# Optimization experiments

Measured on AMD Instinct MI355X. Metric: run time of the kernel, lower is better.

Reference implementation:

```python
import jax, jax.numpy as jnp
import numpy as np

B, N, C, E = 4, 20000, 64, 320000

def setup_inputs() -> dict:
    key = jax.random.key(0)
    ks = jax.random.split(key, 9)
    s = 0.1
    return {
        "x": jax.random.normal(ks[0], (B, N, C), jnp.float32),
        "edge_index": jax.random.randint(ks[1], (2, E), 0, N, jnp.int64),
        "lin_w": jax.random.normal(ks[2], (C, C), jnp.float32) * s,
        "bias": jnp.zeros((C,), jnp.float32),
        "up1_w": jax.random.normal(ks[3], (C, C), jnp.float32) * s,
        "up2_w": jax.random.normal(ks[4], (C, C), jnp.float32) * s,
        "lo1_w": jax.random.normal(ks[5], (C, C), jnp.float32) * s,
        "lo2_w": jax.random.normal(ks[6], (C, C), jnp.float32) * s,
        "last_w": jax.random.normal(ks[7], (2 * C, 2 * C), jnp.float32) * s,
    }

def reference(x, edge_index, lin_w, bias, up1_w, up2_w, lo1_w, lo2_w, last_w):
    n = x.shape[1]
    # add self loops (PyG add_self_loops)
    loops = jnp.arange(n, dtype=edge_index.dtype)
    row = jnp.concatenate([edge_index[0], loops])  # source
    col = jnp.concatenate([edge_index[1], loops])  # target
    # linear transform (Linear with no bias: x @ W^T)
    h = jnp.einsum("bnc,oc->bno", x, lin_w)
    # symmetric degree normalization; degree computed on col (targets)
    deg = jax.ops.segment_sum(jnp.ones_like(col, dtype=h.dtype), col, num_segments=n)
    dis = jnp.where(deg > 0, deg ** -0.5, 0.0)
    norm = dis[row] * dis[col]  # [E+N]
    # gather / scale / scatter-add (GCN propagate with aggr='add')
    msg = h[:, row, :] * norm[None, :, None]          # [B, E+N, C]
    agg = jax.ops.segment_sum(jnp.swapaxes(msg, 0, 1), col, num_segments=n)  # [N, B, C]
    out = jnp.swapaxes(agg, 0, 1) + bias              # [B, N, C]
    fst = jax.nn.sigmoid(out)
    upper = jnp.einsum("bnc,oc->bno", jnp.einsum("bnc,oc->bno", fst, up1_w), up2_w)
    lower = jnp.einsum("bnc,oc->bno", jnp.einsum("bnc,oc->bno", fst, lo1_w), lo2_w)
    combined = jnp.concatenate([upper, lower], axis=2)  # [B, N, 2C]
    last = jnp.einsum("bnc,oc->bno", combined, last_w)
    return jax.nn.relu(last)
```

## Files before the change

kernel.cpp:

```cpp
#include <hip/hip_runtime.h>
#include <cstdint>
#include <cstddef>

#define NODES 20000
#define NEDGE 320000
#define CAP 64
#define NEB 1250
#define LINB 16
#define BIGB 32

using bf16x8 = __attribute__((ext_vector_type(8))) __bf16;
using f32x4  = __attribute__((ext_vector_type(4))) float;
using f32x2  = __attribute__((ext_vector_type(2))) float;

__device__ __forceinline__ unsigned short f2bf(float f) {
  union { float f; unsigned int u; } v; v.f = f;
  unsigned int r = v.u + 0x7FFF + ((v.u >> 16) & 1);
  return (unsigned short)(r >> 16);
}

__global__ void k_build(const int* __restrict__ ei, int* __restrict__ cnt,
                        int* __restrict__ csr,
                        const float* __restrict__ lin, const float* __restrict__ u1,
                        const float* __restrict__ u2, const float* __restrict__ l1,
                        const float* __restrict__ l2, const float* __restrict__ lastw,
                        unsigned short* __restrict__ wb16) {
  __shared__ float tmp_u[4][64];
  __shared__ float tmp_l[4][64];
  int bid = blockIdx.x, t = threadIdx.x;
  if (bid < NEB) {
    int i = bid * 256 + t;
    if (i < NEDGE) {
      int row = ei[i];
      int col = ei[NEDGE + i];
      int pos = atomicAdd(&cnt[col], 1);
      if (pos < CAP) csr[col * CAP + pos] = row;
    }
  } else if (bid < NEB + LINB) {
    int g = (bid - NEB) * 256 + t;
    wb16[g] = f2bf(lin[g]);
  } else {
    int o0 = (bid - NEB - LINB) * 4;
    int ol = t >> 6, p = t & 63;
    float su = 0.f, sl = 0.f;
    for (int k = 0; k < 64; ++k) {
      float lu = lastw[(o0 + ol) * 128 + k];
      float ll = lastw[(o0 + ol) * 128 + 64 + k];
      su += lu * u2[k * 64 + p];
      sl += ll * l2[k * 64 + p];
    }
    tmp_u[ol][p] = su;
    tmp_l[ol][p] = sl;
    __syncthreads();
    int j = p;
    float acc = 0.f;
    for (int q = 0; q < 64; ++q)
      acc += tmp_u[ol][q] * u1[q * 64 + j] + tmp_l[ol][q] * l1[q * 64 + j];
    wb16[4096 + (o0 + ol) * 64 + j] = f2bf(acc);
  }
}

__global__ void k_xconv(const int* __restrict__ cnt, float* __restrict__ dis,
                        const float* __restrict__ x, unsigned int* __restrict__ xs8) {
  int g = blockIdx.x * 256 + threadIdx.x;
  int n = g >> 6, i = g & 63;
  int b = i >> 4, c = (i & 15) * 4;
  float ds = rsqrtf((float)(cnt[n] + 1));
  if (i == 0) dis[n] = ds;
  f32x4 v = __builtin_nontemporal_load(
      (const f32x4*)(x + ((size_t)b * NODES + n) * 64 + c));
  int p = 0;
  p = __builtin_amdgcn_cvt_pk_fp8_f32(v.x * ds, v.y * ds, p, false);
  p = __builtin_amdgcn_cvt_pk_fp8_f32(v.z * ds, v.w * ds, p, true);
  xs8[(size_t)n * 64 + i] = (unsigned int)p;
}

__global__ __launch_bounds__(256) void k_gpost(const int* __restrict__ cnt,
                                               const int* __restrict__ csr,
                                               const unsigned int* __restrict__ xs8,
                                               const float* __restrict__ dis,
                                               const float* __restrict__ bias,
                                               const unsigned short* __restrict__ wb16,
                                               float* __restrict__ out) {
  __shared__ unsigned short xa[32][72];
  __shared__ unsigned short fst[32][72];
  int t = threadIdx.x;
  int w = t >> 6, l = t & 63;
  int n0 = blockIdx.x * 8;

  for (int j = 0; j < 2; ++j) {
    int n = n0 + 2 * w + j;
    int dn = cnt[n]; if (dn > CAP) dn = CAP;
    int beg = n * CAP, end = beg + dn;
    float a0, a1, a2, a3;
    {
      unsigned int u = xs8[(size_t)n * 64 + l];
      f32x2 lo = __builtin_amdgcn_cvt_pk_f32_fp8(u, false);
      f32x2 hi = __builtin_amdgcn_cvt_pk_f32_fp8(u, true);
      a0 = lo.x; a1 = lo.y; a2 = hi.x; a3 = hi.y;
    }
    int i = beg;
    for (; i + 8 <= end; i += 8) {
      int r0 = csr[i],     r1 = csr[i + 1], r2 = csr[i + 2], r3 = csr[i + 3];
      int r4 = csr[i + 4], r5 = csr[i + 5], r6 = csr[i + 6], r7 = csr[i + 7];
      unsigned int u0 = xs8[(size_t)r0 * 64 + l];
      unsigned int u1 = xs8[(size_t)r1 * 64 + l];
      unsigned int u2 = xs8[(size_t)r2 * 64 + l];
      unsigned int u3 = xs8[(size_t)r3 * 64 + l];
      unsigned int u4 = xs8[(size_t)r4 * 64 + l];
      unsigned int u5 = xs8[(size_t)r5 * 64 + l];
      unsigned int u6 = xs8[(size_t)r6 * 64 + l];
      unsigned int u7 = xs8[(size_t)r7 * 64 + l];
#pragma unroll
      for (int e = 0; e < 8; ++e) {
        unsigned int u = e == 0 ? u0 : e == 1 ? u1 : e == 2 ? u2 : e == 3 ? u3
                       : e == 4 ? u4 : e == 5 ? u5 : e == 6 ? u6 : u7;
        f32x2 lo = __builtin_amdgcn_cvt_pk_f32_fp8(u, false);
        f32x2 hi = __builtin_amdgcn_cvt_pk_f32_fp8(u, true);
        a0 += lo.x; a1 += lo.y; a2 += hi.x; a3 += hi.y;
      }
    }
    for (; i < end; ++i) {
      unsigned int u = xs8[(size_t)csr[i] * 64 + l];
      f32x2 lo = __builtin_amdgcn_cvt_pk_f32_fp8(u, false);
      f32x2 hi = __builtin_amdgcn_cvt_pk_f32_fp8(u, true);
      a0 += lo.x; a1 += lo.y; a2 += hi.x; a3 += hi.y;
    }
    ushort4 o;
    o.x = f2bf(a0); o.y = f2bf(a1); o.z = f2bf(a2); o.w = f2bf(a3);
    *(ushort4*)&xa[(2 * w + j) * 4 + (l >> 4)][(l & 15) * 4] = o;
  }
  __syncthreads();

  int m = l & 15, q = l >> 4;
  const unsigned short* wlin = wb16;
  const unsigned short* bigw = wb16 + 4096;

  {
    f32x4 acc1[2] = {{0,0,0,0},{0,0,0,0}};
#pragma unroll
    for (int kk = 0; kk < 2; ++kk) {
      bf16x8 a = *(const bf16x8*)(wlin + (16 * w + m) * 64 + q * 8 + 32 * kk);
#pragma unroll
      for (int nt = 0; nt < 2; ++nt) {
        bf16x8 b = *(const bf16x8*)&xa[16 * nt + m][q * 8 + 32 * kk];
        acc1[nt] = __builtin_amdgcn_mfma_f32_16x16x32_bf16(a, b, acc1[nt], 0, 0, 0);
      }
    }
    float4 b4 = *(const float4*)(bias + 16 * w + 4 * q);
#pragma unroll
    for (int nt = 0; nt < 2; ++nt) {
      int row = 16 * nt + m;
      float ds = dis[n0 + (row >> 2)];
      float v0 = acc1[nt][0] * ds + b4.x;
      float v1 = acc1[nt][1] * ds + b4.y;
      float v2 = acc1[nt][2] * ds + b4.z;
      float v3 = acc1[nt][3] * ds + b4.w;
      ushort4 o;
      o.x = f2bf(1.f / (1.f + __expf(-v0)));
      o.y = f2bf(1.f / (1.f + __expf(-v1)));
      o.z = f2bf(1.f / (1.f + __expf(-v2)));
      o.w = f2bf(1.f / (1.f + __expf(-v3)));
      *(ushort4*)&fst[row][16 * w + 4 * q] = o;
    }
  }
  __syncthreads();

  {
    f32x4 acc2[2][2] = {{{0,0,0,0},{0,0,0,0}},{{0,0,0,0},{0,0,0,0}}};
#pragma unroll
    for (int kk = 0; kk < 2; ++kk) {
#pragma unroll
      for (int nt = 0; nt < 2; ++nt) {
        bf16x8 a = *(const bf16x8*)&fst[16 * nt + m][q * 8 + 32 * kk];
#pragma unroll
        for (int mt = 0; mt < 2; ++mt) {
          bf16x8 b = *(const bf16x8*)(bigw + (32 * w + 16 * mt + m) * 64 + q * 8 + 32 * kk);
          acc2[mt][nt] = __builtin_amdgcn_mfma_f32_16x16x32_bf16(a, b, acc2[mt][nt], 0, 0, 0);
        }
      }
    }
#pragma unroll
    for (int mt = 0; mt < 2; ++mt)
#pragma unroll
      for (int nt = 0; nt < 2; ++nt)
#pragma unroll
        for (int r = 0; r < 4; ++r) {
          int row = 16 * nt + 4 * q + r;
          int n = n0 + (row >> 2), b = row & 3;
          float v = acc2[mt][nt][r];
          out[((size_t)b * NODES + n) * 128 + 32 * w + 16 * mt + m] = v > 0.f ? v : 0.f;
        }
  }
}

extern "C" void kernel_launch(void* const* d_in, const int* in_sizes, int n_in,
                              void* d_out, int out_size, void* d_ws, size_t ws_size,
                              hipStream_t stream) {
  const float* x     = (const float*)d_in[0];
  const int*   ei    = (const int*)d_in[1];
  const float* lin_w = (const float*)d_in[2];
  const float* bias  = (const float*)d_in[3];
  const float* up1   = (const float*)d_in[4];
  const float* up2   = (const float*)d_in[5];
  const float* lo1   = (const float*)d_in[6];
  const float* lo2   = (const float*)d_in[7];
  const float* lastw = (const float*)d_in[8];
  float* out = (float*)d_out;

  char* ws = (char*)d_ws;
  unsigned short* wb16 = (unsigned short*)(ws);
  float* dis        = (float*)(ws + (64 << 10));
  int*   cnt        = (int*)(ws + (192 << 10));
  int*   csr        = (int*)(ws + (1 << 20));
  unsigned int* xs8 = (unsigned int*)(ws + (8 << 20));

  (void)hipMemsetAsync(cnt, 0, NODES * sizeof(int), stream);
  k_build<<<NEB + LINB + BIGB, 256, 0, stream>>>(ei, cnt, csr, lin_w, up1, up2,
                                                 lo1, lo2, lastw, wb16);
  k_xconv<<<NODES / 4, 256, 0, stream>>>(cnt, dis, x, xs8);
  k_gpost<<<NODES / 8, 256, 0, stream>>>(cnt, csr, xs8, dis, bias, wb16, out);
}
```

Before: 148.0 us.

## Fuse x conversion into build kernel and apply source norm in gather

The separate x-to-fp8 conversion kernel is merged into the build kernel, so one launch disappears. To make that possible, x is no longer pre-scaled by the degree norm; the gather instead reads each source's count and applies rsqrt per edge. The CSR now stores 16-bit indices and each edge thread handles two edges. k_gpost uses 512 threads with one node per wave, and outputs use nontemporal stores. The cost is extra cnt loads and rsqrt work per edge in the gather, plus fp8 quantization of x before normalization instead of after.

```diff
diff --git a/kernel.cpp b/kernel.cpp
--- a/kernel.cpp
+++ b/kernel.cpp
@@ -5,13 +5,17 @@
 #define NODES 20000
 #define NEDGE 320000
 #define CAP 64
-#define NEB 1250
+#define SCATB 625
 #define LINB 16
 #define BIGB 32
+#define XCVB 5000
+#define BLDB (SCATB + LINB + BIGB + XCVB)
 
 using bf16x8 = __attribute__((ext_vector_type(8))) __bf16;
 using f32x4  = __attribute__((ext_vector_type(4))) float;
 using f32x2  = __attribute__((ext_vector_type(2))) float;
+using us8    = __attribute__((ext_vector_type(8))) unsigned short;
+using us4    = __attribute__((ext_vector_type(4))) unsigned short;
 
 __device__ __forceinline__ unsigned short f2bf(float f) {
   union { float f; unsigned int u; } v; v.f = f;
@@ -19,28 +23,37 @@
   return (unsigned short)(r >> 16);
 }
 
+#define DECFMA(u, dr, s0, s1, s2, s3)                           \
+  {                                                             \
+    f32x2 lo_ = __builtin_amdgcn_cvt_pk_f32_fp8(u, false);      \
+    f32x2 hi_ = __builtin_amdgcn_cvt_pk_f32_fp8(u, true);       \
+    s0 += dr * lo_.x; s1 += dr * lo_.y;                         \
+    s2 += dr * hi_.x; s3 += dr * hi_.y;                         \
+  }
+
 __global__ void k_build(const int* __restrict__ ei, int* __restrict__ cnt,
-                        int* __restrict__ csr,
+                        unsigned short* __restrict__ csr16,
                         const float* __restrict__ lin, const float* __restrict__ u1,
                         const float* __restrict__ u2, const float* __restrict__ l1,
                         const float* __restrict__ l2, const float* __restrict__ lastw,
-                        unsigned short* __restrict__ wb16) {
+                        unsigned short* __restrict__ wb16,
+                        const float* __restrict__ x, unsigned int* __restrict__ xs8) {
   __shared__ float tmp_u[4][64];
   __shared__ float tmp_l[4][64];
   int bid = blockIdx.x, t = threadIdx.x;
-  if (bid < NEB) {
-    int i = bid * 256 + t;
-    if (i < NEDGE) {
-      int row = ei[i];
-      int col = ei[NEDGE + i];
-      int pos = atomicAdd(&cnt[col], 1);
-      if (pos < CAP) csr[col * CAP + pos] = row;
-    }
-  } else if (bid < NEB + LINB) {
-    int g = (bid - NEB) * 256 + t;
+  if (bid < SCATB) {
+    int i = (bid * 256 + t) * 2;
+    int2 r2 = *(const int2*)(ei + i);
+    int2 c2 = *(const int2*)(ei + NEDGE + i);
+    int p0 = atomicAdd(&cnt[c2.x], 1);
+    if (p0 < CAP) csr16[c2.x * CAP + p0] = (unsigned short)r2.x;
+    int p1 = atomicAdd(&cnt[c2.y], 1);
+    if (p1 < CAP) csr16[c2.y * CAP + p1] = (unsigned short)r2.y;
+  } else if (bid < SCATB + LINB) {
+    int g = (bid - SCATB) * 256 + t;
     wb16[g] = f2bf(lin[g]);
-  } else {
-    int o0 = (bid - NEB - LINB) * 4;
+  } else if (bid < SCATB + LINB + BIGB) {
+    int o0 = (bid - SCATB - LINB) * 4;
     int ol = t >> 6, p = t & 63;
     float su = 0.f, sl = 0.f;
     for (int k = 0; k < 64; ++k) {
@@ -52,33 +65,26 @@
     tmp_u[ol][p] = su;
     tmp_l[ol][p] = sl;
     __syncthreads();
-    int j = p;
     float acc = 0.f;
     for (int q = 0; q < 64; ++q)
-      acc += tmp_u[ol][q] * u1[q * 64 + j] + tmp_l[ol][q] * l1[q * 64 + j];
-    wb16[4096 + (o0 + ol) * 64 + j] = f2bf(acc);
-  }
-}
-
-__global__ void k_xconv(const int* __restrict__ cnt, float* __restrict__ dis,
-                        const float* __restrict__ x, unsigned int* __restrict__ xs8) {
-  int g = blockIdx.x * 256 + threadIdx.x;
-  int n = g >> 6, i = g & 63;
-  int b = i >> 4, c = (i & 15) * 4;
-  float ds = rsqrtf((float)(cnt[n] + 1));
-  if (i == 0) dis[n] = ds;
-  f32x4 v = __builtin_nontemporal_load(
-      (const f32x4*)(x + ((size_t)b * NODES + n) * 64 + c));
-  int p = 0;
-  p = __builtin_amdgcn_cvt_pk_fp8_f32(v.x * ds, v.y * ds, p, false);
-  p = __builtin_amdgcn_cvt_pk_fp8_f32(v.z * ds, v.w * ds, p, true);
-  xs8[(size_t)n * 64 + i] = (unsigned int)p;
-}
-
-__global__ __launch_bounds__(256) void k_gpost(const int* __restrict__ cnt,
-                                               const int* __restrict__ csr,
+      acc += tmp_u[ol][q] * u1[q * 64 + p] + tmp_l[ol][q] * l1[q * 64 + p];
+    wb16[4096 + (o0 + ol) * 64 + p] = f2bf(acc);
+  } else {
+    int g = (bid - SCATB - LINB - BIGB) * 256 + t;
+    int n = g >> 6, i = g & 63;
+    int b = i >> 4, c = (i & 15) * 4;
+    f32x4 v = __builtin_nontemporal_load(
+        (const f32x4*)(x + ((size_t)b * NODES + n) * 64 + c));
+    int p = 0;
+    p = __builtin_amdgcn_cvt_pk_fp8_f32(v.x, v.y, p, false);
+    p = __builtin_amdgcn_cvt_pk_fp8_f32(v.z, v.w, p, true);
+    xs8[(size_t)n * 64 + i] = (unsigned int)p;
+  }
+}
+
+__global__ __launch_bounds__(512) void k_gpost(const int* __restrict__ cnt,
+                                               const unsigned short* __restrict__ csr16,
                                                const unsigned int* __restrict__ xs8,
-                                               const float* __restrict__ dis,
                                                const float* __restrict__ bias,
                                                const unsigned short* __restrict__ wb16,
                                                float* __restrict__ out) {
@@ -87,110 +93,147 @@
   int t = threadIdx.x;
   int w = t >> 6, l = t & 63;
   int n0 = blockIdx.x * 8;
-
-  for (int j = 0; j < 2; ++j) {
-    int n = n0 + 2 * w + j;
-    int dn = cnt[n]; if (dn > CAP) dn = CAP;
-    int beg = n * CAP, end = beg + dn;
-    float a0, a1, a2, a3;
-    {
-      unsigned int u = xs8[(size_t)n * 64 + l];
-      f32x2 lo = __builtin_amdgcn_cvt_pk_f32_fp8(u, false);
-      f32x2 hi = __builtin_amdgcn_cvt_pk_f32_fp8(u, true);
-      a0 = lo.x; a1 = lo.y; a2 = hi.x; a3 = hi.y;
-    }
-    int i = beg;
-    for (; i + 8 <= end; i += 8) {
-      int r0 = csr[i],     r1 = csr[i + 1], r2 = csr[i + 2], r3 = csr[i + 3];
-      int r4 = csr[i + 4], r5 = csr[i + 5], r6 = csr[i + 6], r7 = csr[i + 7];
-      unsigned int u0 = xs8[(size_t)r0 * 64 + l];
-      unsigned int u1 = xs8[(size_t)r1 * 64 + l];
-      unsigned int u2 = xs8[(size_t)r2 * 64 + l];
-      unsigned int u3 = xs8[(size_t)r3 * 64 + l];
-      unsigned int u4 = xs8[(size_t)r4 * 64 + l];
-      unsigned int u5 = xs8[(size_t)r5 * 64 + l];
-      unsigned int u6 = xs8[(size_t)r6 * 64 + l];
-      unsigned int u7 = xs8[(size_t)r7 * 64 + l];
-#pragma unroll
-      for (int e = 0; e < 8; ++e) {
-        unsigned int u = e == 0 ? u0 : e == 1 ? u1 : e == 2 ? u2 : e == 3 ? u3
-                       : e == 4 ? u4 : e == 5 ? u5 : e == 6 ? u6 : u7;
-        f32x2 lo = __builtin_amdgcn_cvt_pk_f32_fp8(u, false);
-        f32x2 hi = __builtin_amdgcn_cvt_pk_f32_fp8(u, true);
-        a0 += lo.x; a1 += lo.y; a2 += hi.x; a3 += hi.y;
-      }
-    }
-    for (; i < end; ++i) {
-      unsigned int u = xs8[(size_t)csr[i] * 64 + l];
-      f32x2 lo = __builtin_amdgcn_cvt_pk_f32_fp8(u, false);
-      f32x2 hi = __builtin_amdgcn_cvt_pk_f32_fp8(u, true);
-      a0 += lo.x; a1 += lo.y; a2 += hi.x; a3 += hi.y;
-    }
+  int n = n0 + w;
+
+  int cn = cnt[n];
+  int dn = cn > CAP ? CAP : cn;
+  float dsn = rsqrtf((float)(cn + 1));
+
+  float a0, a1, a2, a3;
+  {
+    unsigned int u = xs8[(size_t)n * 64 + l];
+    f32x2 lo = __builtin_amdgcn_cvt_pk_f32_fp8(u, false);
+    f32x2 hi = __builtin_amdgcn_cvt_pk_f32_fp8(u, true);
+    a0 = dsn * lo.x; a1 = dsn * lo.y; a2 = dsn * hi.x; a3 = dsn * hi.y;
+  }
+
+  int base = n * CAP, i = 0;
+  for (; i + 8 <= dn; i += 8) {
+    us8 r8 = __builtin_nontemporal_load((const us8*)(csr16 + base + i));
+    int r0 = r8[0], r1 = r8[1], r2 = r8[2], r3 = r8[3];
+    int r4 = r8[4], r5 = r8[5], r6 = r8[6], r7 = r8[7];
+    int c0 = cnt[r0], c1 = cnt[r1], c2 = cnt[r2], c3 = cnt[r3];
+    int c4 = cnt[r4], c5 = cnt[r5], c6 = cnt[r6], c7 = cnt[r7];
+    unsigned int u0 = xs8[(size_t)r0 * 64 + l];
+    unsigned int u1 = xs8[(size_t)r1 * 64 + l];
+    unsigned int u2 = xs8[(size_t)r2 * 64 + l];
+    unsigned int u3 = xs8[(size_t)r3 * 64 + l];
+    unsigned int u4 = xs8[(size_t)r4 * 64 + l];
+    unsigned int u5 = xs8[(size_t)r5 * 64 + l];
+    unsigned int u6 = xs8[(size_t)r6 * 64 + l];
+    unsigned int u7 = xs8[(size_t)r7 * 64 + l];
+    float d0 = rsqrtf((float)(c0 + 1)), d1 = rsqrtf((float)(c1 + 1));
+    float d2 = rsqrtf((float)(c2 + 1)), d3 = rsqrtf((float)(c3 + 1));
+    float d4 = rsqrtf((float)(c4 + 1)), d5 = rsqrtf((float)(c5 + 1));
+    float d6 = rsqrtf((float)(c6 + 1)), d7 = rsqrtf((float)(c7 + 1));
+    DECFMA(u0, d0, a0, a1, a2, a3); DECFMA(u1, d1, a0, a1, a2, a3);
+    DECFMA(u2, d2, a0, a1, a2, a3); DECFMA(u3, d3, a0, a1, a2, a3);
+    DECFMA(u4, d4, a0, a1, a2, a3); DECFMA(u5, d5, a0, a1, a2, a3);
+    DECFMA(u6, d6, a0, a1, a2, a3); DECFMA(u7, d7, a0, a1, a2, a3);
+  }
+  if (i + 4 <= dn) {
+    us4 r4v = __builtin_nontemporal_load((const us4*)(csr16 + base + i));
+    int r0 = r4v[0], r1 = r4v[1], r2 = r4v[2], r3 = r4v[3];
+    int c0 = cnt[r0], c1 = cnt[r1], c2 = cnt[r2], c3 = cnt[r3];
+    unsigned int u0 = xs8[(size_t)r0 * 64 + l];
+    unsigned int u1 = xs8[(size_t)r1 * 64 + l];
+    unsigned int u2 = xs8[(size_t)r2 * 64 + l];
+    unsigned int u3 = xs8[(size_t)r3 * 64 + l];
+    float d0 = rsqrtf((float)(c0 + 1)), d1 = rsqrtf((float)(c1 + 1));
+    float d2 = rsqrtf((float)(c2 + 1)), d3 = rsqrtf((float)(c3 + 1));
+    DECFMA(u0, d0, a0, a1, a2, a3); DECFMA(u1, d1, a0, a1, a2, a3);
+    DECFMA(u2, d2, a0, a1, a2, a3); DECFMA(u3, d3, a0, a1, a2, a3);
+    i += 4;
+  }
+  for (; i < dn; ++i) {
+    int r = csr16[base + i];
+    float dr = rsqrtf((float)(cnt[r] + 1));
+    unsigned int u = xs8[(size_t)r * 64 + l];
+    DECFMA(u, dr, a0, a1, a2, a3);
+  }
+
+  {
     ushort4 o;
     o.x = f2bf(a0); o.y = f2bf(a1); o.z = f2bf(a2); o.w = f2bf(a3);
-    *(ushort4*)&xa[(2 * w + j) * 4 + (l >> 4)][(l & 15) * 4] = o;
-  }
-  __syncthreads();
+    *(ushort4*)&xa[w * 4 + (l >> 4)][(l & 15) * 4] = o;
+  }
 
   int m = l & 15, q = l >> 4;
   const unsigned short* wlin = wb16;
   const unsigned short* bigw = wb16 + 4096;
-
-  {
-    f32x4 acc1[2] = {{0,0,0,0},{0,0,0,0}};
-#pragma unroll
-    for (int kk = 0; kk < 2; ++kk) {
-      bf16x8 a = *(const bf16x8*)(wlin + (16 * w + m) * 64 + q * 8 + 32 * kk);
-#pragma unroll
-      for (int nt = 0; nt < 2; ++nt) {
-        bf16x8 b = *(const bf16x8*)&xa[16 * nt + m][q * 8 + 32 * kk];
-        acc1[nt] = __builtin_amdgcn_mfma_f32_16x16x32_bf16(a, b, acc1[nt], 0, 0, 0);
-      }
-    }
-    float4 b4 = *(const float4*)(bias + 16 * w + 4 * q);
-#pragma unroll
-    for (int nt = 0; nt < 2; ++nt) {
-      int row = 16 * nt + m;
-      float ds = dis[n0 + (row >> 2)];
-      float v0 = acc1[nt][0] * ds + b4.x;
-      float v1 = acc1[nt][1] * ds + b4.y;
-      float v2 = acc1[nt][2] * ds + b4.z;
-      float v3 = acc1[nt][3] * ds + b4.w;
+  int ws1 = w & 3;
+
+  bf16x8 wa0 = *(const bf16x8*)(wlin + (16 * ws1 + m) * 64 + q * 8);
+  bf16x8 wa1 = *(const bf16x8*)(wlin + (16 * ws1 + m) * 64 + q * 8 + 32);
+  bf16x8 wbk0 = *(const bf16x8*)(bigw + (16 * w + m) * 64 + q * 8);
+  bf16x8 wbk1 = *(const bf16x8*)(bigw + (16 * w + m) * 64 + q * 8 + 32);
+  float4 b4 = *(const float4*)(bias + 16 * ws1 + 4 * q);
+  float ds0 = rsqrtf((float)(cnt[n0 + (m >> 2)] + 1));
+  float ds1 = rsqrtf((float)(cnt[n0 + 4 + (m >> 2)] + 1));
+
+  __syncthreads();
+
+  if (w < 4) {
+    f32x4 acc10 = {0, 0, 0, 0}, acc11 = {0, 0, 0, 0};
+    bf16x8 x00 = *(const bf16x8*)&xa[m][q * 8];
+    bf16x8 x10 = *(const bf16x8*)&xa[16 + m][q * 8];
+    acc10 = __builtin_amdgcn_mfma_f32_16x16x32_bf16(wa0, x00, acc10, 0, 0, 0);
+    acc11 = __builtin_amdgcn_mfma_f32_16x16x32_bf16(wa0, x10, acc11, 0, 0, 0);
+    bf16x8 x01 = *(const bf16x8*)&xa[m][q * 8 + 32];
+    bf16x8 x11 = *(const bf16x8*)&xa[16 + m][q * 8 + 32];
+    acc10 = __builtin_amdgcn_mfma_f32_16x16x32_bf16(wa1, x01, acc10, 0, 0, 0);
+    acc11 = __builtin_amdgcn_mfma_f32_16x16x32_bf16(wa1, x11, acc11, 0, 0, 0);
+    {
+      float v0 = acc10[0] * ds0 + b4.x;
+      float v1 = acc10[1] * ds0 + b4.y;
+      float v2 = acc10[2] * ds0 + b4.z;
+      float v3 = acc10[3] * ds0 + b4.w;
       ushort4 o;
       o.x = f2bf(1.f / (1.f + __expf(-v0)));
       o.y = f2bf(1.f / (1.f + __expf(-v1)));
       o.z = f2bf(1.f / (1.f + __expf(-v2)));
       o.w = f2bf(1.f / (1.f + __expf(-v3)));
-      *(ushort4*)&fst[row][16 * w + 4 * q] = o;
+      *(ushort4*)&fst[m][16 * ws1 + 4 * q] = o;
+    }
+    {
+      float v0 = acc11[0] * ds1 + b4.x;
+      float v1 = acc11[1] * ds1 + b4.y;
+      float v2 = acc11[2] * ds1 + b4.z;
+      float v3 = acc11[3] * ds1 + b4.w;
+      ushort4 o;
+      o.x = f2bf(1.f / (1.f + __expf(-v0)));
+      o.y = f2bf(1.f / (1.f + __expf(-v1)));
+      o.z = f2bf(1.f / (1.f + __expf(-v2)));
+      o.w = f2bf(1.f / (1.f + __expf(-v3)));
+      *(ushort4*)&fst[16 + m][16 * ws1 + 4 * q] = o;
     }
   }
   __syncthreads();
 
   {
-    f32x4 acc2[2][2] = {{{0,0,0,0},{0,0,0,0}},{{0,0,0,0},{0,0,0,0}}};
+    f32x4 a00 = {0, 0, 0, 0}, a01 = {0, 0, 0, 0};
+    bf16x8 f00 = *(const bf16x8*)&fst[m][q * 8];
+    bf16x8 f10 = *(const bf16x8*)&fst[16 + m][q * 8];
+    a00 = __builtin_amdgcn_mfma_f32_16x16x32_bf16(f00, wbk0, a00, 0, 0, 0);
+    a01 = __builtin_amdgcn_mfma_f32_16x16x32_bf16(f10, wbk0, a01, 0, 0, 0);
+    bf16x8 f01 = *(const bf16x8*)&fst[m][q * 8 + 32];
+    bf16x8 f11 = *(const bf16x8*)&fst[16 + m][q * 8 + 32];
+    a00 = __builtin_amdgcn_mfma_f32_16x16x32_bf16(f01, wbk1, a00, 0, 0, 0);
+    a01 = __builtin_amdgcn_mfma_f32_16x16x32_bf16(f11, wbk1, a01, 0, 0, 0);
+
 #pragma unroll
-    for (int kk = 0; kk < 2; ++kk) {
+    for (int nt = 0; nt < 2; ++nt) {
+      f32x4 acc = nt == 0 ? a00 : a01;
 #pragma unroll
-      for (int nt = 0; nt < 2; ++nt) {
-        bf16x8 a = *(const bf16x8*)&fst[16 * nt + m][q * 8 + 32 * kk];
-#pragma unroll
-        for (int mt = 0; mt < 2; ++mt) {
-          bf16x8 b = *(const bf16x8*)(bigw + (32 * w + 16 * mt + m) * 64 + q * 8 + 32 * kk);
-          acc2[mt][nt] = __builtin_amdgcn_mfma_f32_16x16x32_bf16(a, b, acc2[mt][nt], 0, 0, 0);
-        }
+      for (int r = 0; r < 4; ++r) {
+        int row = 16 * nt + 4 * q + r;
+        int nn = n0 + (row >> 2), b = row & 3;
+        float v = acc[r];
+        __builtin_nontemporal_store(
+            v > 0.f ? v : 0.f,
+            out + ((size_t)b * NODES + nn) * 128 + 16 * w + m);
       }
     }
-#pragma unroll
-    for (int mt = 0; mt < 2; ++mt)
-#pragma unroll
-      for (int nt = 0; nt < 2; ++nt)
-#pragma unroll
-        for (int r = 0; r < 4; ++r) {
-          int row = 16 * nt + 4 * q + r;
-          int n = n0 + (row >> 2), b = row & 3;
-          float v = acc2[mt][nt][r];
-          out[((size_t)b * NODES + n) * 128 + 32 * w + 16 * mt + m] = v > 0.f ? v : 0.f;
-        }
   }
 }
 
@@ -209,15 +252,13 @@
   float* out = (float*)d_out;
 
   char* ws = (char*)d_ws;
-  unsigned short* wb16 = (unsigned short*)(ws);
-  float* dis        = (float*)(ws + (64 << 10));
-  int*   cnt        = (int*)(ws + (192 << 10));
-  int*   csr        = (int*)(ws + (1 << 20));
-  unsigned int* xs8 = (unsigned int*)(ws + (8 << 20));
+  unsigned short* wb16  = (unsigned short*)(ws);
+  int*            cnt   = (int*)(ws + (192 << 10));
+  unsigned short* csr16 = (unsigned short*)(ws + (1 << 20));
+  unsigned int*   xs8   = (unsigned int*)(ws + (8 << 20));
 
   (void)hipMemsetAsync(cnt, 0, NODES * sizeof(int), stream);
-  k_build<<<NEB + LINB + BIGB, 256, 0, stream>>>(ei, cnt, csr, lin_w, up1, up2,
-                                                 lo1, lo2, lastw, wb16);
-  k_xconv<<<NODES / 4, 256, 0, stream>>>(cnt, dis, x, xs8);
-  k_gpost<<<NODES / 8, 256, 0, stream>>>(cnt, csr, xs8, dis, bias, wb16, out);
-}
+  k_build<<<BLDB, 256, 0, stream>>>(ei, cnt, csr16, lin_w, up1, up2, lo1, lo2,
+                                    lastw, wb16, x, xs8);
+  k_gpost<<<NODES / 8, 512, 0, stream>>>(cnt, csr16, xs8, bias, wb16, out);
+}
```

New measurement: 139.1 us. 6.0% less time.
